# Performance work log

Measured on AMD Instinct MI355X. Metric: run time of the kernel, lower is better.

Reference implementation:

```python
import jax, jax.numpy as jnp
import numpy as np

# Physical constants (normalized units, CFL-stable: c*dt/dx = 0.5)
DX = 0.01
DT = 0.005
C = 1.0
EPSILON = 1.0

def _make_kernels():
    # D02: second derivative along last axis (x); D20 = transpose (y)
    d02 = np.array([[0.0, 0.0, 0.0],
                    [1.0, -2.0, 1.0],
                    [0.0, 0.0, 0.0]], dtype=np.float32) / (DX * DX)
    d20 = d02.T
    # OIHW, single in/out channel
    return jnp.asarray(d02)[None, None], jnp.asarray(d20)[None, None]

_D02, _D20 = _make_kernels()

def _conv3x3(u, k):
    # same padding, stride 1, NCHW
    return jax.lax.conv_general_dilated(
        u, k, window_strides=(1, 1), padding=[(1, 1), (1, 1)],
        dimension_numbers=('NCHW', 'OIHW', 'NCHW'))

def setup_inputs() -> dict:
    key = jax.random.key(0)
    k1, k2, k3, k4 = jax.random.split(key, 4)
    B, H, W = 16, 1024, 1024
    shp = (B, 1, H, W)
    return {
        'u1': jax.random.normal(k1, shp, dtype=jnp.float32),
        'u0': jax.random.normal(k2, shp, dtype=jnp.float32),
        'j2': jax.random.normal(k3, shp, dtype=jnp.float32),
        'j0': jax.random.normal(k4, shp, dtype=jnp.float32),
    }

def reference(u1, u0, j2, j0):
    D20u1 = _conv3x3(u1, _D20)  # d^2/dy^2
    D02u1 = _conv3x3(u1, _D02)  # d^2/dx^2
    u2 = (2.0 * u1 - u0
          + (DT * DT) * (C * C) * (D20u1 + D02u1)
          - (DT / (2.0 * EPSILON)) * (j2 - j0))
    return u2
```

## Files before the change

kernel.cpp:

```cpp
#include <hip/hip_runtime.h>

#define WIDTH  1024
#define HEIGHT 1024

__global__ __launch_bounds__(256) void fdtd_kernel(
    const float* __restrict__ u1,
    const float* __restrict__ u0,
    const float* __restrict__ j2,
    const float* __restrict__ j0,
    float* __restrict__ out,
    int nrows)
{
    const int row = blockIdx.x;
    if (row >= nrows) return;
    const int y  = row & (HEIGHT - 1);
    const int x0 = threadIdx.x << 2;
    const long base = (long)row * WIDTH + x0;

    const float4 c   = *(const float4*)(u1 + base);
    const float4 a0  = *(const float4*)(u0 + base);
    const float4 b2  = *(const float4*)(j2 + base);
    const float4 b0  = *(const float4*)(j0 + base);
    float4 up = make_float4(0.f, 0.f, 0.f, 0.f);
    float4 dn = make_float4(0.f, 0.f, 0.f, 0.f);
    if (y > 0)          up = *(const float4*)(u1 + base - WIDTH);
    if (y < HEIGHT - 1) dn = *(const float4*)(u1 + base + WIDTH);

    const float left  = (x0 > 0)         ? u1[base - 1] : 0.0f;
    const float right = (x0 + 4 < WIDTH) ? u1[base + 4] : 0.0f;

    const float cf[4]  = {c.x,  c.y,  c.z,  c.w};
    const float u0f[4] = {a0.x, a0.y, a0.z, a0.w};
    const float j2f[4] = {b2.x, b2.y, b2.z, b2.w};
    const float j0f[4] = {b0.x, b0.y, b0.z, b0.w};
    const float upf[4] = {up.x, up.y, up.z, up.w};
    const float dnf[4] = {dn.x, dn.y, dn.z, dn.w};

    float o[4];
#pragma unroll
    for (int i = 0; i < 4; ++i) {
        const float l = (i == 0) ? left  : cf[i - 1];
        const float r = (i == 3) ? right : cf[i + 1];
        const float lap = upf[i] + dnf[i] + l + r - 4.0f * cf[i];
        o[i] = 2.0f * cf[i] - u0f[i]
             + 0.25f * lap
             - 0.0025f * (j2f[i] - j0f[i]);
    }
    *(float4*)(out + base) = make_float4(o[0], o[1], o[2], o[3]);
}

extern "C" void kernel_launch(void* const* d_in, const int* in_sizes, int n_in,
                              void* d_out, int out_size, void* d_ws, size_t ws_size,
                              hipStream_t stream) {
    const float* u1 = (const float*)d_in[0];
    const float* u0 = (const float*)d_in[1];
    const float* j2 = (const float*)d_in[2];
    const float* j0 = (const float*)d_in[3];
    float* out = (float*)d_out;

    const int nrows = out_size / WIDTH;
    dim3 block(WIDTH / 4);
    dim3 grid(nrows);
    fdtd_kernel<<<grid, block, 0, stream>>>(u1, u0, j2, j0, out, nrows);
}
```

Before: 251.5 us.

## Process eight rows per block with register-rolled vertical reuse and wave shuffles

```diff
diff --git a/kernel.cpp b/kernel.cpp
--- a/kernel.cpp
+++ b/kernel.cpp
@@ -2,51 +2,50 @@
 
 #define WIDTH  1024
 #define HEIGHT 1024
+#define ROWS_PER_BLOCK 8
 
 __global__ __launch_bounds__(256) void fdtd_kernel(
     const float* __restrict__ u1,
     const float* __restrict__ u0,
     const float* __restrict__ j2,
     const float* __restrict__ j0,
-    float* __restrict__ out,
-    int nrows)
+    float* __restrict__ out)
 {
-    const int row = blockIdx.x;
-    if (row >= nrows) return;
-    const int y  = row & (HEIGHT - 1);
-    const int x0 = threadIdx.x << 2;
-    const long base = (long)row * WIDTH + x0;
+    const int row0 = blockIdx.x * ROWS_PER_BLOCK;
+    const int y0   = row0 & (HEIGHT - 1);
+    const int lane = threadIdx.x & 63;
+    const int x0   = threadIdx.x << 2;
+    long base = (long)row0 * WIDTH + x0;
 
-    const float4 c   = *(const float4*)(u1 + base);
-    const float4 a0  = *(const float4*)(u0 + base);
-    const float4 b2  = *(const float4*)(j2 + base);
-    const float4 b0  = *(const float4*)(j0 + base);
-    float4 up = make_float4(0.f, 0.f, 0.f, 0.f);
-    float4 dn = make_float4(0.f, 0.f, 0.f, 0.f);
-    if (y > 0)          up = *(const float4*)(u1 + base - WIDTH);
-    if (y < HEIGHT - 1) dn = *(const float4*)(u1 + base + WIDTH);
+    const float4 zero = make_float4(0.f, 0.f, 0.f, 0.f);
 
-    const float left  = (x0 > 0)         ? u1[base - 1] : 0.0f;
-    const float right = (x0 + 4 < WIDTH) ? u1[base + 4] : 0.0f;
+    float4 up = (y0 > 0) ? *(const float4*)(u1 + base - WIDTH) : zero;
+    float4 c  = *(const float4*)(u1 + base);
 
-    const float cf[4]  = {c.x,  c.y,  c.z,  c.w};
-    const float u0f[4] = {a0.x, a0.y, a0.z, a0.w};
-    const float j2f[4] = {b2.x, b2.y, b2.z, b2.w};
-    const float j0f[4] = {b0.x, b0.y, b0.z, b0.w};
-    const float upf[4] = {up.x, up.y, up.z, up.w};
-    const float dnf[4] = {dn.x, dn.y, dn.z, dn.w};
+#pragma unroll
+    for (int r = 0; r < ROWS_PER_BLOCK; ++r) {
+        const int y = y0 + r;
+        const float4 dn = (y < HEIGHT - 1) ? *(const float4*)(u1 + base + WIDTH) : zero;
+        const float4 a0 = *(const float4*)(u0 + base);
+        const float4 b2 = *(const float4*)(j2 + base);
+        const float4 b0 = *(const float4*)(j0 + base);
 
-    float o[4];
-#pragma unroll
-    for (int i = 0; i < 4; ++i) {
-        const float l = (i == 0) ? left  : cf[i - 1];
-        const float r = (i == 3) ? right : cf[i + 1];
-        const float lap = upf[i] + dnf[i] + l + r - 4.0f * cf[i];
-        o[i] = 2.0f * cf[i] - u0f[i]
-             + 0.25f * lap
-             - 0.0025f * (j2f[i] - j0f[i]);
+        float left  = __shfl_up(c.w, 1);
+        float right = __shfl_down(c.x, 1);
+        if (lane == 0)  left  = (x0 > 0)         ? u1[base - 1] : 0.0f;
+        if (lane == 63) right = (x0 + 4 < WIDTH) ? u1[base + 4] : 0.0f;
+
+        float4 o;
+        o.x = 2.0f * c.x - a0.x + 0.25f * (up.x + dn.x + left + c.y - 4.0f * c.x) - 0.0025f * (b2.x - b0.x);
+        o.y = 2.0f * c.y - a0.y + 0.25f * (up.y + dn.y + c.x  + c.z - 4.0f * c.y) - 0.0025f * (b2.y - b0.y);
+        o.z = 2.0f * c.z - a0.z + 0.25f * (up.z + dn.z + c.y  + c.w - 4.0f * c.z) - 0.0025f * (b2.z - b0.z);
+        o.w = 2.0f * c.w - a0.w + 0.25f * (up.w + dn.w + c.z  + right - 4.0f * c.w) - 0.0025f * (b2.w - b0.w);
+        *(float4*)(out + base) = o;
+
+        up = c;
+        c  = dn;
+        base += WIDTH;
     }
-    *(float4*)(out + base) = make_float4(o[0], o[1], o[2], o[3]);
 }
 
 extern "C" void kernel_launch(void* const* d_in, const int* in_sizes, int n_in,
@@ -60,6 +59,6 @@
 
     const int nrows = out_size / WIDTH;
     dim3 block(WIDTH / 4);
-    dim3 grid(nrows);
-    fdtd_kernel<<<grid, block, 0, stream>>>(u1, u0, j2, j0, out, nrows);
+    dim3 grid(nrows / ROWS_PER_BLOCK);
+    fdtd_kernel<<<grid, block, 0, stream>>>(u1, u0, j2, j0, out);
 }
```

Result: slower. 260.7 us (+3.6%).
